# Kernel tuning notes

Hardware: AMD Instinct MI355X
Metric: run time of the kernel (lower is better)

## Reference

```python
import jax, jax.numpy as jnp
import numpy as np

B, T, C = 8, 4096, 192
HIMG, WIMG = 64, 64
NH, HS = 24, 8
MIX_DIM, DECAY_DIM = 32, 64


def _conv2d(x, w, pad):
    # x: [B, C, H, W], w: [Cout, Cin, kh, kw]
    return jax.lax.conv_general_dilated(
        x, w, (1, 1), [(pad, pad), (pad, pad)],
        dimension_numbers=('NCHW', 'OIHW', 'NCHW'))


def setup_inputs() -> dict:
    key = jax.random.key(0)
    ks = jax.random.split(key, 26)
    f = jax.random.normal
    s = 1.0 / np.sqrt(C)
    return {
        'x': f(ks[0], (B, T, C), jnp.float32),
        'maa_x': f(ks[1], (1, 1, C), jnp.float32) * 0.1,
        'maa_w': f(ks[2], (1, 1, C), jnp.float32) * 0.1,
        'maa_k': f(ks[3], (1, 1, C), jnp.float32) * 0.1,
        'maa_v': f(ks[4], (1, 1, C), jnp.float32) * 0.1,
        'maa_r': f(ks[5], (1, 1, C), jnp.float32) * 0.1,
        'maa_g': f(ks[6], (1, 1, C), jnp.float32) * 0.1,
        'maa_w1': f(ks[7], (C, 5 * MIX_DIM), jnp.float32) * 0.01,
        'maa_w2': f(ks[8], (5, MIX_DIM, C), jnp.float32) * 0.01,
        'decay_w1': f(ks[9], (C, DECAY_DIM), jnp.float32) * 0.01,
        'decay_w2': f(ks[10], (DECAY_DIM, C), jnp.float32) * 0.01,
        'spatial_decay': f(ks[11], (1, 1, C), jnp.float32) * 0.5,
        'u': f(ks[12], (NH, HS), jnp.float32) * 0.5,
        'Wr': f(ks[13], (C, C), jnp.float32) * s,
        'Wk': f(ks[14], (C, C), jnp.float32) * s,
        'Wv': f(ks[15], (C, C), jnp.float32) * s,
        'Wg': f(ks[16], (C, C), jnp.float32) * s,
        'Wo': f(ks[17], (C, C), jnp.float32) * s,
        'ln_g': jnp.ones((C,), jnp.float32),
        'ln_b': jnp.zeros((C,), jnp.float32),
        'w_lp': f(ks[18], (C, C), jnp.float32) * s,
        'w_hd': f(ks[19], (C, C, 3), jnp.float32) * s,
        'w_vd': f(ks[20], (C, C, 3), jnp.float32) * s,
        'w_cd': f(ks[21], (C, C, 3, 3), jnp.float32) * (s / 3.0),
        'theta_cd': jnp.full((1,), 0.7, jnp.float32),
    }


def _diff_conv_mix(x2d, w_lp, w_hd, w_vd, w_cd, theta_cd):
    Cc = x2d.shape[1]
    # laplacian-pattern conv from a 1x1 weight (Conv2d_lp)
    k9 = jnp.zeros((Cc, Cc, 9), x2d.dtype)
    k9 = k9.at[:, :, jnp.array([1, 3, 5, 7])].set(w_lp[:, :, None])
    k9 = k9.at[:, :, 4].set(-4.0 * w_lp)
    out = _conv2d(x2d, k9.reshape(Cc, Cc, 3, 3), 1)
    # horizontal difference conv (Conv2d_hd)
    k9 = jnp.zeros((Cc, Cc, 9), x2d.dtype)
    k9 = k9.at[:, :, jnp.array([0, 3, 6])].set(w_hd)
    k9 = k9.at[:, :, jnp.array([2, 5, 8])].set(-w_hd)
    out = out + _conv2d(x2d, k9.reshape(Cc, Cc, 3, 3), 1)
    # vertical difference conv (Conv2d_vd)
    k9 = jnp.zeros((Cc, Cc, 9), x2d.dtype)
    k9 = k9.at[:, :, jnp.array([0, 1, 2])].set(w_vd)
    k9 = k9.at[:, :, jnp.array([6, 7, 8])].set(-w_vd)
    out = out + _conv2d(x2d, k9.reshape(Cc, Cc, 3, 3), 1)
    # central difference conv (Conv2d_cd): normal conv + 1x1 (-theta * kernel sum)
    out = out + _conv2d(x2d, w_cd, 1)
    kd = jnp.sum(w_cd, axis=(2, 3), keepdims=True) * (-theta_cd[0])
    out = out + _conv2d(x2d, kd, 0)
    return out


def reference(x, maa_x, maa_w, maa_k, maa_v, maa_r, maa_g, maa_w1, maa_w2,
              decay_w1, decay_w2, spatial_decay, u, Wr, Wk, Wv, Wg, Wo,
              ln_g, ln_b, w_lp, w_hd, w_vd, w_cd, theta_cd):
    Bb, Tt, Cc = x.shape
    x2d = x.transpose(0, 2, 1).reshape(Bb, Cc, HIMG, WIMG)
    shifted = _diff_conv_mix(x2d, w_lp, w_hd, w_vd, w_cd, theta_cd)
    xx = shifted.reshape(Bb, Cc, Tt).transpose(0, 2, 1) - x  # spatial shift delta

    # data-dependent token mixing (RWKV6 maa)
    xxx = x + xx * maa_x
    tmp = jnp.tanh(xxx @ maa_w1).reshape(Bb, Tt, 5, MIX_DIM)
    m = jnp.einsum('btfd,fdc->fbtc', tmp, maa_w2)  # [5, B, T, C]
    mw, mk, mv, mr, mg = m[0], m[1], m[2], m[3], m[4]
    xw = x + xx * (maa_w + mw)
    xk = x + xx * (maa_k + mk)
    xv = x + xx * (maa_v + mv)
    xr = x + xx * (maa_r + mr)
    xg = x + xx * (maa_g + mg)

    r = xr @ Wr
    k = xk @ Wk
    v = xv @ Wv
    g = jax.nn.silu(xg @ Wg)
    w = spatial_decay + jnp.tanh(xw @ decay_w1) @ decay_w2  # [B, T, C]

    # WKV6 linear recurrence, fp32 state, per-head [HS, HS]
    rh = r.reshape(Bb, Tt, NH, HS).astype(jnp.float32)
    kh = k.reshape(Bb, Tt, NH, HS).astype(jnp.float32)
    vh = v.reshape(Bb, Tt, NH, HS).astype(jnp.float32)
    dh = jnp.exp(-jnp.exp(w.astype(jnp.float32))).reshape(Bb, Tt, NH, HS)
    uf = u.astype(jnp.float32)

    def step(S, inp):  # S: [B, NH, HS(j key), HS(i value)]
        rt, kt, vt, dt = inp  # each [B, NH, HS]
        kv = kt[..., :, None] * vt[..., None, :]
        yt = jnp.einsum('bhj,bhji->bhi', rt, S + uf[None, :, :, None] * kv)
        return dt[..., None] * S + kv, yt

    xs = tuple(a.transpose(1, 0, 2, 3) for a in (rh, kh, vh, dh))  # time-major
    S0 = jnp.zeros((Bb, NH, HS, HS), jnp.float32)
    _, ys = jax.lax.scan(step, S0, xs)
    y = ys.transpose(1, 0, 2, 3).reshape(Bb, Tt, Cc).astype(x.dtype)

    # ln_x then gated output projection
    mu = jnp.mean(y, axis=-1, keepdims=True)
    var = jnp.mean((y - mu) ** 2, axis=-1, keepdims=True)
    yn = (y - mu) * jax.lax.rsqrt(var + 1e-5) * ln_g + ln_b
    return (yn * g) @ Wo
```

## Files before the change

kernel.cpp:

```cpp
#include <hip/hip_runtime.h>
#include <hip/hip_bf16.h>

#define Bq 8
#define Tq 4096
#define Cq 192
#define NHq 24
#define HSq 8
#define Mq (Bq * Tq)

#define CLq 64
#define NCHq (Tq / CLq)
#define TSq 32

typedef short short8 __attribute__((ext_vector_type(8)));
typedef float f32x4 __attribute__((ext_vector_type(4)));

__device__ __forceinline__ unsigned short f2bf(float f) {
    union { float f; unsigned u; } v; v.f = f;
    unsigned u = v.u;
    return (unsigned short)((u + 0x7FFFu + ((u >> 16) & 1u)) >> 16);
}
__device__ __forceinline__ float bf2f(unsigned short u) {
    union { unsigned u; float f; } v; v.u = (unsigned)u << 16;
    return v.f;
}
__device__ __forceinline__ float4 bf4_to_f4(ushort4 u) {
    return make_float4(bf2f(u.x), bf2f(u.y), bf2f(u.z), bf2f(u.w));
}

__global__ void prep_weights_kernel(const float* __restrict__ w_lp,
                                    const float* __restrict__ w_hd,
                                    const float* __restrict__ w_vd,
                                    const float* __restrict__ w_cd,
                                    const float* __restrict__ theta,
                                    unsigned short* __restrict__ Wg) {
    int idx = blockIdx.x * 256 + threadIdx.x;
    if (idx >= Cq * Cq) return;
    int cout = idx / Cq, cin = idx - cout * Cq;
    float t9[9];
#pragma unroll
    for (int t = 0; t < 9; ++t) t9[t] = 0.f;
    float lp = w_lp[idx];
    t9[1] += lp; t9[3] += lp; t9[5] += lp; t9[7] += lp; t9[4] -= 4.f * lp;
    float h0 = w_hd[idx * 3 + 0], h1 = w_hd[idx * 3 + 1], h2 = w_hd[idx * 3 + 2];
    t9[0] += h0; t9[3] += h1; t9[6] += h2;
    t9[2] -= h0; t9[5] -= h1; t9[8] -= h2;
    float v0 = w_vd[idx * 3 + 0], v1 = w_vd[idx * 3 + 1], v2 = w_vd[idx * 3 + 2];
    t9[0] += v0; t9[1] += v1; t9[2] += v2;
    t9[6] -= v0; t9[7] -= v1; t9[8] -= v2;
    float sum = 0.f;
#pragma unroll
    for (int t = 0; t < 9; ++t) {
        float cdv = w_cd[idx * 9 + t];
        t9[t] += cdv; sum += cdv;
    }
    t9[4] -= theta[0] * sum;
#pragma unroll
    for (int t = 0; t < 9; ++t)
        Wg[(size_t)cout * 1728 + t * Cq + cin] = f2bf(t9[t]);
}

__global__ __launch_bounds__(256) void prep_pack_kernel(
    const float* __restrict__ maa_w1, const float* __restrict__ Wr,
    const float* __restrict__ Wk, const float* __restrict__ Wv,
    const float* __restrict__ Wgp, const float* __restrict__ Wo,
    const float* __restrict__ maa_w2, const float* __restrict__ d1,
    const float* __restrict__ d2,
    unsigned short* __restrict__ Wt_maa, unsigned short* __restrict__ Wt_r,
    unsigned short* __restrict__ Wt_k, unsigned short* __restrict__ Wt_v,
    unsigned short* __restrict__ Wt_g, unsigned short* __restrict__ Wt_o,
    unsigned short* __restrict__ w2t, unsigned short* __restrict__ Wt_d1,
    unsigned short* __restrict__ Wt_d2) {
    int idx = blockIdx.x * 256 + threadIdx.x;
    if (idx < 30720) {
        int n = idx / 192, k = idx - n * 192;
        Wt_maa[idx] = f2bf(maa_w1[(size_t)k * 160 + n]);
        return;
    }
    idx -= 30720;
    if (idx < 5 * 36864) {
        int s = idx / 36864, e = idx - s * 36864;
        int n = e / 192, k = e - n * 192;
        const float* W = s == 0 ? Wr : s == 1 ? Wk : s == 2 ? Wv : s == 3 ? Wgp : Wo;
        unsigned short* D = s == 0 ? Wt_r : s == 1 ? Wt_k : s == 2 ? Wt_v : s == 3 ? Wt_g : Wt_o;
        D[e] = f2bf(W[(size_t)k * 192 + n]);
        return;
    }
    idx -= 5 * 36864;
    if (idx < 30720) {
        int f = idx / 6144, rem = idx - f * 6144;
        int n = rem >> 5, k = rem & 31;
        w2t[idx] = f2bf(maa_w2[(size_t)(f * 32 + k) * 192 + n]);
        return;
    }
    idx -= 30720;
    if (idx < 12288) {
        int n = idx / 192, k = idx - n * 192;
        Wt_d1[idx] = f2bf(d1[(size_t)k * 64 + n]);
        return;
    }
    idx -= 12288;
    if (idx < 12288) {
        int n = idx / 64, k = idx - n * 64;
        Wt_d2[idx] = f2bf(d2[(size_t)k * 192 + n]);
    }
}

__global__ __launch_bounds__(256) void halo_kernel(
    const float* __restrict__ x, unsigned short* __restrict__ xh) {
    int idx = blockIdx.x * 256 + threadIdx.x;
    int c4 = (idx % 48) * 4;
    int cell = idx / 48;
    int hx = cell % 66;
    int rest = cell / 66;
    int hy = rest % 66;
    int bb = rest / 66;
    ushort4 o = make_ushort4(0, 0, 0, 0);
    if (hy >= 1 && hy <= 64 && hx >= 1 && hx <= 64) {
        size_t g = ((size_t)(bb << 12) + (hy - 1) * 64 + (hx - 1)) * Cq + c4;
        float4 v = *(const float4*)&x[g];
        o = make_ushort4(f2bf(v.x), f2bf(v.y), f2bf(v.z), f2bf(v.w));
    }
    *(ushort4*)&xh[(size_t)cell * Cq + c4] = o;
}

#define GBM 128
#define GBK 64

template <int ALOAD, int EPI, int OBF16, int BN>
__global__ __launch_bounds__(256) void mgemm_kernel(
    const unsigned short* __restrict__ Asrc,
    const unsigned short* __restrict__ Wt,
    void* __restrict__ Cv, int N, int K,
    const float* __restrict__ aux0,
    const unsigned short* __restrict__ xh,
    unsigned short* __restrict__ C2) {
    __shared__ unsigned char lds[(GBM + BN) * GBK * 2];
    unsigned char* Alds = lds;
    unsigned char* Blds = lds + GBM * GBK * 2;
    float* C = (float*)Cv;
    unsigned short* Cb = (unsigned short*)Cv;

    const int tid = threadIdx.x;
    const int wid = tid >> 6, lane = tid & 63;
    const int llo = lane & 15, lhi = lane >> 4;
    const int m0 = blockIdx.x * GBM, n0 = blockIdx.y * BN;
    const int NF = BN / 16;

    f32x4 acc[2][BN / 16];
#pragma unroll
    for (int a = 0; a < 2; ++a)
#pragma unroll
        for (int b = 0; b < NF; ++b) {
            f32x4 z = {0.f, 0.f, 0.f, 0.f};
            acc[a][b] = z;
        }

    for (int k0 = 0; k0 < K; k0 += GBK) {
        __syncthreads();
#pragma unroll
        for (int rep = 0; rep < 4; ++rep) {
            int c = tid + rep * 256;
            int row = c >> 3, kseg = c & 7;
            int m = m0 + row;
            short8 val;
            if (ALOAD == 3) {
                val = *(const short8*)&Asrc[(size_t)m * K + k0 + kseg * 8];
            } else {
                int tap = k0 / Cq;
                int cinb = k0 - tap * Cq;
                int t3 = tap / 3;
                int bb = m >> 12, pos = m & 4095;
                int hy = (pos >> 6) + t3;
                int hx = (pos & 63) + tap - t3 * 3;
                size_t g = ((size_t)bb * 4356 + hy * 66 + hx) * Cq + cinb + kseg * 8;
                val = *(const short8*)&Asrc[g];
            }
            *(short8*)(Alds + row * 128 + ((kseg * 16) ^ ((row & 7) << 4))) = val;
        }
#pragma unroll
        for (int rep = 0; rep < BN / 32; ++rep) {
            int c = tid + rep * 256;
            int row = c >> 3, kseg = c & 7;
            int n = n0 + row;
            short8 val = {0, 0, 0, 0, 0, 0, 0, 0};
            if (n < N) val = *(const short8*)&Wt[(size_t)n * K + k0 + kseg * 8];
            *(short8*)(Blds + row * 128 + ((kseg * 16) ^ ((row & 7) << 4))) = val;
        }
        __syncthreads();
#pragma unroll
        for (int kc = 0; kc < 2; ++kc) {
            int kb = kc * 64 + lhi * 16;
            short8 af[2], bq[BN / 16];
#pragma unroll
            for (int mf = 0; mf < 2; ++mf) {
                int row = wid * 32 + mf * 16 + llo;
                af[mf] = *(const short8*)(Alds + row * 128 + (kb ^ ((row & 7) << 4)));
            }
#pragma unroll
            for (int nf = 0; nf < NF; ++nf) {
                int row = nf * 16 + llo;
                bq[nf] = *(const short8*)(Blds + row * 128 + (kb ^ ((row & 7) << 4)));
            }
#pragma unroll
            for (int mf = 0; mf < 2; ++mf)
#pragma unroll
                for (int nf = 0; nf < NF; ++nf)
                    acc[mf][nf] = __builtin_amdgcn_mfma_f32_16x16x32_bf16(
                        af[mf], bq[nf], acc[mf][nf], 0, 0, 0);
        }
    }
    if (EPI == 5) {
#pragma unroll
        for (int mf = 0; mf < 2; ++mf)
#pragma unroll
            for (int nf = 0; nf < NF; ++nf) {
                int n = n0 + nf * 16 + llo;
#pragma unroll
                for (int r = 0; r < 4; ++r) {
                    int m = m0 + wid * 32 + mf * 16 + lhi * 4 + r;
                    int pos = m & 4095, bb = m >> 12;
                    size_t cell = (size_t)bb * 4356 + ((pos >> 6) + 1) * 66 + (pos & 63) + 1;
                    float xv = bf2f(xh[cell * Cq + n]);
                    float xxv = acc[mf][nf][r] - xv;
                    Cb[(size_t)m * Cq + n] = f2bf(xxv);
                    C2[(size_t)m * Cq + n] = f2bf(fmaf(xxv, aux0[n], xv));
                }
            }
        return;
    }
#pragma unroll
    for (int mf = 0; mf < 2; ++mf) {
#pragma unroll
        for (int nf = 0; nf < NF; ++nf) {
            int n = n0 + nf * 16 + llo;
            if (n >= N) continue;
#pragma unroll
            for (int r = 0; r < 4; ++r) {
                int m = m0 + wid * 32 + mf * 16 + lhi * 4 + r;
                float val = acc[mf][nf][r];
                if (EPI == 2) val = tanhf(val);
                else if (EPI == 4) val = expf(-expf(aux0[n] + val));
                if (OBF16) Cb[(size_t)m * N + n] = f2bf(val);
                else C[(size_t)m * N + n] = val;
            }
        }
    }
}

__global__ __launch_bounds__(256) void proj4_kernel(
    const unsigned short* __restrict__ A0, const unsigned short* __restrict__ A1,
    const unsigned short* __restrict__ A2, const unsigned short* __restrict__ A3,
    const unsigned short* __restrict__ W0, const unsigned short* __restrict__ W1,
    const unsigned short* __restrict__ W2, const unsigned short* __restrict__ W3,
    unsigned short* __restrict__ O0, unsigned short* __restrict__ O1,
    unsigned short* __restrict__ O2, unsigned short* __restrict__ O3) {
    __shared__ unsigned char lds[(GBM + 64) * GBK * 2];
    unsigned char* Alds = lds;
    unsigned char* Blds = lds + GBM * GBK * 2;
    const int z = blockIdx.z;
    const unsigned short* Asrc = z == 0 ? A0 : z == 1 ? A1 : z == 2 ? A2 : A3;
    const unsigned short* Wt = z == 0 ? W0 : z == 1 ? W1 : z == 2 ? W2 : W3;
    unsigned short* Cb = z == 0 ? O0 : z == 1 ? O1 : z == 2 ? O2 : O3;
    const bool silu = (z == 3);

    const int tid = threadIdx.x;
    const int wid = tid >> 6, lane = tid & 63;
    const int llo = lane & 15, lhi = lane >> 4;
    const int m0 = blockIdx.x * GBM, n0 = blockIdx.y * 64;

    f32x4 acc[2][4];
#pragma unroll
    for (int a = 0; a < 2; ++a)
#pragma unroll
        for (int b = 0; b < 4; ++b) {
            f32x4 zz = {0.f, 0.f, 0.f, 0.f};
            acc[a][b] = zz;
        }

    for (int k0 = 0; k0 < Cq; k0 += GBK) {
        __syncthreads();
#pragma unroll
        for (int rep = 0; rep < 4; ++rep) {
            int c = tid + rep * 256;
            int row = c >> 3, kseg = c & 7;
            short8 val = *(const short8*)&Asrc[(size_t)(m0 + row) * Cq + k0 + kseg * 8];
            *(short8*)(Alds + row * 128 + ((kseg * 16) ^ ((row & 7) << 4))) = val;
        }
#pragma unroll
        for (int rep = 0; rep < 2; ++rep) {
            int c = tid + rep * 256;
            int row = c >> 3, kseg = c & 7;
            short8 val = *(const short8*)&Wt[(size_t)(n0 + row) * Cq + k0 + kseg * 8];
            *(short8*)(Blds + row * 128 + ((kseg * 16) ^ ((row & 7) << 4))) = val;
        }
        __syncthreads();
#pragma unroll
        for (int kc = 0; kc < 2; ++kc) {
            int kb = kc * 64 + lhi * 16;
            short8 af[2], bq[4];
#pragma unroll
            for (int mf = 0; mf < 2; ++mf) {
                int row = wid * 32 + mf * 16 + llo;
                af[mf] = *(const short8*)(Alds + row * 128 + (kb ^ ((row & 7) << 4)));
            }
#pragma unroll
            for (int nf = 0; nf < 4; ++nf) {
                int row = nf * 16 + llo;
                bq[nf] = *(const short8*)(Blds + row * 128 + (kb ^ ((row & 7) << 4)));
            }
#pragma unroll
            for (int mf = 0; mf < 2; ++mf)
#pragma unroll
                for (int nf = 0; nf < 4; ++nf)
                    acc[mf][nf] = __builtin_amdgcn_mfma_f32_16x16x32_bf16(
                        af[mf], bq[nf], acc[mf][nf], 0, 0, 0);
        }
    }
#pragma unroll
    for (int mf = 0; mf < 2; ++mf)
#pragma unroll
        for (int nf = 0; nf < 4; ++nf) {
            int n = n0 + nf * 16 + llo;
#pragma unroll
            for (int r = 0; r < 4; ++r) {
                int m = m0 + wid * 32 + mf * 16 + lhi * 4 + r;
                float val = acc[mf][nf][r];
                if (silu) val = val / (1.f + expf(-val));
                Cb[(size_t)m * Cq + n] = f2bf(val);
            }
        }
}

#define MLDW 72
__global__ __launch_bounds__(128) void mix5_kernel(
    const unsigned short* __restrict__ xh,
    const unsigned short* __restrict__ xxb,
    const unsigned short* __restrict__ tmp_bf,
    const unsigned short* __restrict__ w2t,
    const float* __restrict__ maa_w, const float* __restrict__ maa_k,
    const float* __restrict__ maa_v, const float* __restrict__ maa_r,
    const float* __restrict__ maa_g,
    unsigned short* __restrict__ xw, unsigned short* __restrict__ xr,
    unsigned short* __restrict__ xk, unsigned short* __restrict__ xv,
    unsigned short* __restrict__ xg) {
    __shared__ unsigned short tile[2][5][16][MLDW];
    const int tid = threadIdx.x;
    const int wid = tid >> 6, lane = tid & 63;
    const int llo = lane & 15, lhi = lane >> 4;
    const int mb = blockIdx.x * 64 + wid * 32;
    const int nb = blockIdx.y * 64;

    short8 aw[5][4];
#pragma unroll
    for (int f = 0; f < 5; ++f)
#pragma unroll
        for (int nf = 0; nf < 4; ++nf)
            aw[f][nf] = *(const short8*)&w2t[((size_t)f * Cq + nb + nf * 16 + llo) * 32 + lhi * 8];

    unsigned short* const outs[5] = {xw, xk, xv, xr, xg};

#pragma unroll
    for (int sub = 0; sub < 2; ++sub) {
        short8 bt[5];
        {
            const unsigned short* trow = &tmp_bf[(size_t)(mb + sub * 16 + llo) * 160 + lhi * 8];
#pragma unroll
            for (int f = 0; f < 5; ++f) bt[f] = *(const short8*)&trow[f * 32];
        }
        int m = mb + sub * 16 + llo;
        int pos = m & 4095, bb = m >> 12;
        size_t xbase = ((size_t)bb * 4356 + ((pos >> 6) + 1) * 66 + (pos & 63) + 1) * Cq;
#pragma unroll
        for (int nf = 0; nf < 4; ++nf) {
            f32x4 acc[5];
#pragma unroll
            for (int f = 0; f < 5; ++f) {
                f32x4 z = {0.f, 0.f, 0.f, 0.f};
                acc[f] = __builtin_amdgcn_mfma_f32_16x16x32_bf16(aw[f][nf], bt[f], z, 0, 0, 0);
            }
            int n0 = nb + nf * 16 + lhi * 4;
            size_t g = (size_t)m * Cq + n0;
            float4 xv4 = bf4_to_f4(*(const ushort4*)&xh[xbase + n0]);
            float4 xx4 = bf4_to_f4(*(const ushort4*)&xxb[g]);
            float4 mw4 = *(const float4*)&maa_w[n0];
            float4 mk4 = *(const float4*)&maa_k[n0];
            float4 mv4 = *(const float4*)&maa_v[n0];
            float4 mr4 = *(const float4*)&maa_r[n0];
            float4 mg4 = *(const float4*)&maa_g[n0];
            float xvv[4] = {xv4.x, xv4.y, xv4.z, xv4.w};
            float xxv[4] = {xx4.x, xx4.y, xx4.z, xx4.w};
            float mwv[4] = {mw4.x, mw4.y, mw4.z, mw4.w};
            float mkv[4] = {mk4.x, mk4.y, mk4.z, mk4.w};
            float mvv[4] = {mv4.x, mv4.y, mv4.z, mv4.w};
            float mrv[4] = {mr4.x, mr4.y, mr4.z, mr4.w};
            float mgv[4] = {mg4.x, mg4.y, mg4.z, mg4.w};
            ushort4 ov[5];
#pragma unroll
            for (int r = 0; r < 4; ++r) {
                ((unsigned short*)&ov[0])[r] = f2bf(fmaf(xxv[r], mwv[r] + acc[0][r], xvv[r]));
                ((unsigned short*)&ov[1])[r] = f2bf(fmaf(xxv[r], mkv[r] + acc[1][r], xvv[r]));
                ((unsigned short*)&ov[2])[r] = f2bf(fmaf(xxv[r], mvv[r] + acc[2][r], xvv[r]));
                ((unsigned short*)&ov[3])[r] = f2bf(fmaf(xxv[r], mrv[r] + acc[3][r], xvv[r]));
                ((unsigned short*)&ov[4])[r] = f2bf(fmaf(xxv[r], mgv[r] + acc[4][r], xvv[r]));
            }
            int col = nf * 16 + lhi * 4;
#pragma unroll
            for (int f = 0; f < 5; ++f)
                *(ushort4*)&tile[wid][f][llo][col] = ov[f];
        }
        int row16 = lane >> 3;
        int colc = (lane & 7) * 8;
#pragma unroll
        for (int f = 0; f < 5; ++f) {
#pragma unroll
            for (int p = 0; p < 2; ++p) {
                int rr = p * 8 + row16;
                int gm = mb + sub * 16 + rr;
                *(short8*)&outs[f][(size_t)gm * Cq + nb + colc] =
                    *(const short8*)&tile[wid][f][rr][colc];
            }
        }
    }
}

__global__ __launch_bounds__(64) void wkv_pass1_kernel(
    const unsigned short* __restrict__ k, const unsigned short* __restrict__ v,
    const float* __restrict__ d,
    float* __restrict__ Dbuf, float* __restrict__ Cbuf) {
    int chunk = blockIdx.x, hg = blockIdx.y, b = blockIdx.z;
    int lane = threadIdx.x;
    int slot = lane >> 3, i = lane & 7;
    int cbase = hg * 64;
    size_t gbase = ((size_t)b * Tq + (size_t)chunk * CLq) * Cq + cbase;
    __shared__ float ks[TSq][64], vs[TSq][64], ds[TSq][64];
    float S[8], D[8];
#pragma unroll
    for (int j = 0; j < 8; ++j) { S[j] = 0.f; D[j] = 1.f; }
    for (int t0 = 0; t0 < CLq; t0 += TSq) {
        int f = lane & 15, r4 = lane >> 4;
#pragma unroll
        for (int p = 0; p < 8; ++p) {
            int row = r4 + p * 4;
            size_t g = gbase + (size_t)(t0 + row) * Cq + f * 4;
            *(float4*)&ks[row][f * 4] = bf4_to_f4(*(const ushort4*)&k[g]);
            *(float4*)&vs[row][f * 4] = bf4_to_f4(*(const ushort4*)&v[g]);
            *(float4*)&ds[row][f * 4] = *(const float4*)&d[g];
        }
        __syncthreads();
#pragma unroll 8
        for (int t = 0; t < TSq; ++t) {
            float vv = vs[t][lane];
            float4 ka = *(const float4*)&ks[t][slot * 8];
            float4 kb = *(const float4*)&ks[t][slot * 8 + 4];
            float4 da = *(const float4*)&ds[t][slot * 8];
            float4 db = *(const float4*)&ds[t][slot * 8 + 4];
            float kk[8] = {ka.x, ka.y, ka.z, ka.w, kb.x, kb.y, kb.z, kb.w};
            float dd[8] = {da.x, da.y, da.z, da.w, db.x, db.y, db.z, db.w};
#pragma unroll
            for (int j = 0; j < 8; ++j) {
                float kv = kk[j] * vv;
                S[j] = fmaf(dd[j], S[j], kv);
                D[j] *= dd[j];
            }
        }
        __syncthreads();
    }
    size_t dbase = (((size_t)b * NCHq + chunk) * NHq + hg * 8) * 8;
    Dbuf[dbase + lane] = D[i];
    size_t cb = (((size_t)b * NCHq + chunk) * NHq + (hg * 8 + slot)) * 64 + i;
#pragma unroll
    for (int j = 0; j < 8; ++j) Cbuf[cb + j * 8] = S[j];
}

__global__ __launch_bounds__(64) void wkv_pass2_kernel(
    const float* __restrict__ Dbuf, const float* __restrict__ Cbuf,
    float* __restrict__ Sbuf) {
    int bh = blockIdx.x;
    int lane = threadIdx.x;
    int j = lane >> 3, i = lane & 7;
    int b = bh / NHq, h = bh - b * NHq;
    float S = 0.f;
    size_t stride = (size_t)NHq * 64;
    size_t base = ((size_t)b * NCHq * NHq + h) * 64 + j * 8 + i;
    size_t dstride = (size_t)NHq * 8;
    size_t dbase = ((size_t)b * NCHq * NHq + h) * 8 + j;
#pragma unroll 4
    for (int c = 0; c < NCHq; ++c) {
        Sbuf[base + c * stride] = S;
        float D = Dbuf[dbase + c * dstride];
        float C = Cbuf[base + c * stride];
        S = fmaf(D, S, C);
    }
}

__global__ __launch_bounds__(64) void wkv_pass3_kernel(
    const unsigned short* __restrict__ r, const unsigned short* __restrict__ k,
    const unsigned short* __restrict__ v, const float* __restrict__ d,
    const float* __restrict__ u, const float* __restrict__ Sbuf,
    unsigned short* __restrict__ y) {
    int chunk = blockIdx.x, hg = blockIdx.y, b = blockIdx.z;
    int lane = threadIdx.x;
    int slot = lane >> 3, i = lane & 7;
    int h = hg * 8 + slot;
    int cbase = hg * 64;
    size_t gbase = ((size_t)b * Tq + (size_t)chunk * CLq) * Cq + cbase;
    __shared__ float rs[TSq][64], ks[TSq][64], vs[TSq][64], ds[TSq][64];
    float S[8], uu[8];
    size_t sb = (((size_t)b * NCHq + chunk) * NHq + h) * 64 + i;
#pragma unroll
    for (int j = 0; j < 8; ++j) {
        S[j] = Sbuf[sb + j * 8];
        uu[j] = u[h * 8 + j];
    }
    for (int t0 = 0; t0 < CLq; t0 += TSq) {
        int f = lane & 15, r4 = lane >> 4;
#pragma unroll
        for (int p = 0; p < 8; ++p) {
            int row = r4 + p * 4;
            size_t g = gbase + (size_t)(t0 + row) * Cq + f * 4;
            *(float4*)&rs[row][f * 4] = bf4_to_f4(*(const ushort4*)&r[g]);
            *(float4*)&ks[row][f * 4] = bf4_to_f4(*(const ushort4*)&k[g]);
            *(float4*)&vs[row][f * 4] = bf4_to_f4(*(const ushort4*)&v[g]);
            *(float4*)&ds[row][f * 4] = *(const float4*)&d[g];
        }
        __syncthreads();
#pragma unroll 8
        for (int t = 0; t < TSq; ++t) {
            float vv = vs[t][lane];
            float4 ra = *(const float4*)&rs[t][slot * 8];
            float4 rb = *(const float4*)&rs[t][slot * 8 + 4];
            float4 ka = *(const float4*)&ks[t][slot * 8];
            float4 kb = *(const float4*)&ks[t][slot * 8 + 4];
            float4 da = *(const float4*)&ds[t][slot * 8];
            float4 db = *(const float4*)&ds[t][slot * 8 + 4];
            float rr[8] = {ra.x, ra.y, ra.z, ra.w, rb.x, rb.y, rb.z, rb.w};
            float kk[8] = {ka.x, ka.y, ka.z, ka.w, kb.x, kb.y, kb.z, kb.w};
            float dd[8] = {da.x, da.y, da.z, da.w, db.x, db.y, db.z, db.w};
            float yv = 0.f;
#pragma unroll
            for (int j = 0; j < 8; ++j) {
                float kv = kk[j] * vv;
                yv = fmaf(rr[j], fmaf(uu[j], kv, S[j]), yv);
                S[j] = fmaf(dd[j], S[j], kv);
            }
            y[gbase + (size_t)(t0 + t) * Cq + lane] = f2bf(yv);
        }
        __syncthreads();
    }
}

__global__ __launch_bounds__(256) void ln_gate_kernel(
    const unsigned short* __restrict__ y, const unsigned short* __restrict__ g,
    const float* __restrict__ ln_g, const float* __restrict__ ln_b,
    unsigned short* __restrict__ out) {
    int row = blockIdx.x * 4 + (threadIdx.x >> 6);
    int lane = threadIdx.x & 63;
    const unsigned short* yr = y + (size_t)row * Cq;
    float a0 = bf2f(yr[lane]), a1 = bf2f(yr[lane + 64]), a2 = bf2f(yr[lane + 128]);
    float s = a0 + a1 + a2;
    float ss = a0 * a0 + a1 * a1 + a2 * a2;
#pragma unroll
    for (int m = 1; m < 64; m <<= 1) {
        s += __shfl_xor(s, m);
        ss += __shfl_xor(ss, m);
    }
    float mu = s * (1.f / 192.f);
    float var = ss * (1.f / 192.f) - mu * mu;
    float rstd = rsqrtf(var + 1e-5f);
    const unsigned short* gr = g + (size_t)row * Cq;
    unsigned short* orow = out + (size_t)row * Cq;
    float aa[3] = {a0, a1, a2};
#pragma unroll
    for (int q = 0; q < 3; ++q) {
        int cc = lane + q * 64;
        float yn = (aa[q] - mu) * rstd * ln_g[cc] + ln_b[cc];
        orow[cc] = f2bf(yn * bf2f(gr[cc]));
    }
}

extern "C" void kernel_launch(void* const* d_in, const int* in_sizes, int n_in,
                              void* d_out, int out_size, void* d_ws, size_t ws_size,
                              hipStream_t stream) {
    const float* x        = (const float*)d_in[0];
    const float* maa_x    = (const float*)d_in[1];
    const float* maa_w    = (const float*)d_in[2];
    const float* maa_k    = (const float*)d_in[3];
    const float* maa_v    = (const float*)d_in[4];
    const float* maa_r    = (const float*)d_in[5];
    const float* maa_g    = (const float*)d_in[6];
    const float* maa_w1   = (const float*)d_in[7];
    const float* maa_w2   = (const float*)d_in[8];
    const float* decay_w1 = (const float*)d_in[9];
    const float* decay_w2 = (const float*)d_in[10];
    const float* sdecay   = (const float*)d_in[11];
    const float* u        = (const float*)d_in[12];
    const float* Wr       = (const float*)d_in[13];
    const float* Wk       = (const float*)d_in[14];
    const float* Wv       = (const float*)d_in[15];
    const float* Wgp      = (const float*)d_in[16];
    const float* Wo       = (const float*)d_in[17];
    const float* ln_g     = (const float*)d_in[18];
    const float* ln_b     = (const float*)d_in[19];
    const float* w_lp     = (const float*)d_in[20];
    const float* w_hd     = (const float*)d_in[21];
    const float* w_vd     = (const float*)d_in[22];
    const float* w_cd     = (const float*)d_in[23];
    const float* theta    = (const float*)d_in[24];
    float* out = (float*)d_out;

    const size_t BIG = (size_t)Mq * Cq;
    float* ws = (float*)d_ws;
    unsigned short* Wgt_conv = (unsigned short*)ws;
    unsigned short* Wt_maa = Wgt_conv + (size_t)Cq * 1728;
    unsigned short* Wt_r = Wt_maa + 160 * Cq;
    unsigned short* Wt_k = Wt_r + Cq * Cq;
    unsigned short* Wt_v = Wt_k + Cq * Cq;
    unsigned short* Wt_g = Wt_v + Cq * Cq;
    unsigned short* Wt_o = Wt_g + Cq * Cq;
    unsigned short* w2t  = Wt_o + Cq * Cq;
    unsigned short* Wt_d1 = w2t + 5 * 192 * 32;
    unsigned short* Wt_d2 = Wt_d1 + 64 * Cq;
    float* tmp  = ws + 331776;
    float* wtmp = tmp + (size_t)Mq * 160;
    float* buf0 = wtmp + (size_t)Mq * 64;
    float* buf1 = buf0 + BIG;
    float* buf2 = buf1 + BIG;
    float* buf3 = buf2 + BIG;
    float* buf4 = buf3 + BIG;
    float* buf5 = buf4 + BIG;

    unsigned short* tmp_bf = (unsigned short*)tmp;
    float* Dbuf = tmp + (size_t)Mq * 80;
    float* Cbuf = Dbuf + (size_t)Bq * NCHq * NHq * 8;
    float* Sbuf = Cbuf + (size_t)Bq * NCHq * NHq * 64;

    unsigned short* x_halo = (unsigned short*)buf1;
    unsigned short* y_b    = (unsigned short*)buf1;
    unsigned short* k_b    = (unsigned short*)(buf1 + BIG / 2);
    unsigned short* xx_b   = (unsigned short*)buf0;
    unsigned short* xw_b   = (unsigned short*)(buf0 + BIG / 2);
    unsigned short* r_b    = (unsigned short*)buf0;
    unsigned short* xxx_b  = (unsigned short*)(buf2 + BIG / 2);
    unsigned short* xg_b   = xxx_b;
    unsigned short* xv_b   = (unsigned short*)buf2;
    unsigned short* gate_b = (unsigned short*)buf2;
    unsigned short* v_b    = (unsigned short*)buf3;
    unsigned short* g_b    = (unsigned short*)buf4;
    unsigned short* xr_b   = (unsigned short*)buf5;
    unsigned short* xk_b   = (unsigned short*)(buf5 + BIG / 2);
    float* d_f             = buf5;
    unsigned short* wtmp_b = (unsigned short*)wtmp;

    dim3 blk(256);
    const unsigned short* nosrc = nullptr;
    unsigned short* nodst = nullptr;

    prep_weights_kernel<<<dim3(144), blk, 0, stream>>>(w_lp, w_hd, w_vd, w_cd, theta, Wgt_conv);
    prep_pack_kernel<<<dim3(1056), blk, 0, stream>>>(
        maa_w1, Wr, Wk, Wv, Wgp, Wo, maa_w2, decay_w1, decay_w2,
        Wt_maa, Wt_r, Wt_k, Wt_v, Wt_g, Wt_o, w2t, Wt_d1, Wt_d2);
    halo_kernel<<<dim3(8 * 66 * 66 * 48 / 256), blk, 0, stream>>>(x, x_halo);
    mgemm_kernel<1, 5, 1, 96><<<dim3(Mq / GBM, 2), blk, 0, stream>>>(
        x_halo, Wgt_conv, xx_b, Cq, 1728, maa_x, x_halo, xxx_b);
    mgemm_kernel<3, 2, 1, 64><<<dim3(Mq / GBM, 3), blk, 0, stream>>>(
        xxx_b, Wt_maa, tmp_bf, 160, Cq, nullptr, nosrc, nodst);
    mix5_kernel<<<dim3(Mq / 64, 3), dim3(128), 0, stream>>>(
        x_halo, xx_b, tmp_bf, w2t, maa_w, maa_k, maa_v, maa_r, maa_g,
        xw_b, xr_b, xk_b, xv_b, xg_b);
    proj4_kernel<<<dim3(Mq / GBM, 3, 4), blk, 0, stream>>>(
        xv_b, xr_b, xk_b, xg_b,
        Wt_v, Wt_r, Wt_k, Wt_g,
        v_b, r_b, k_b, g_b);
    mgemm_kernel<3, 2, 1, 64><<<dim3(Mq / GBM, 1), blk, 0, stream>>>(
        xw_b, Wt_d1, wtmp_b, 64, Cq, nullptr, nosrc, nodst);
    mgemm_kernel<3, 4, 0, 64><<<dim3(Mq / GBM, 3), blk, 0, stream>>>(
        wtmp_b, Wt_d2, d_f, Cq, 64, sdecay, nosrc, nodst);
    wkv_pass1_kernel<<<dim3(NCHq, 3, Bq), dim3(64), 0, stream>>>(k_b, v_b, d_f, Dbuf, Cbuf);
    wkv_pass2_kernel<<<dim3(Bq * NHq), dim3(64), 0, stream>>>(Dbuf, Cbuf, Sbuf);
    wkv_pass3_kernel<<<dim3(NCHq, 3, Bq), dim3(64), 0, stream>>>(r_b, k_b, v_b, d_f, u, Sbuf, y_b);
    ln_gate_kernel<<<dim3(Mq / 4), blk, 0, stream>>>(y_b, g_b, ln_g, ln_b, gate_b);
    mgemm_kernel<3, 0, 0, 64><<<dim3(Mq / GBM, 3), blk, 0, stream>>>(
        gate_b, Wt_o, out, Cq, Cq, nullptr, nosrc, nodst);
}
```

Before: 329.1 us.

## Load GEMM A fragments directly from global; keep bf16 in WKV shared memory

The GEMM kernels (mgemm and proj4) no longer stage the A tile through LDS. Each wave loads its MFMA A fragments straight from global memory into registers, and only the weight tile stays in shared memory. The conv GEMM drops its BN=96 template variant and runs as a 3-column grid of 64-wide N tiles. The WKV pass1 and pass3 kernels now keep r, k and v as bf16 in LDS and convert at use, halving their shared-memory footprint and store traffic. The aims are less LDS traffic, fewer LDS stores and better occupancy, at the risk of less coalesced global loads for A and more A re-reads across N tiles.

```diff
diff --git a/kernel.cpp b/kernel.cpp
--- a/kernel.cpp
+++ b/kernel.cpp
@@ -127,7 +127,7 @@
 #define GBM 128
 #define GBK 64
 
-template <int ALOAD, int EPI, int OBF16, int BN>
+template <int ALOAD, int EPI, int OBF16>
 __global__ __launch_bounds__(256) void mgemm_kernel(
     const unsigned short* __restrict__ Asrc,
     const unsigned short* __restrict__ Wt,
@@ -135,23 +135,20 @@
     const float* __restrict__ aux0,
     const unsigned short* __restrict__ xh,
     unsigned short* __restrict__ C2) {
-    __shared__ unsigned char lds[(GBM + BN) * GBK * 2];
-    unsigned char* Alds = lds;
-    unsigned char* Blds = lds + GBM * GBK * 2;
+    __shared__ unsigned char Blds[64 * GBK * 2];
     float* C = (float*)Cv;
     unsigned short* Cb = (unsigned short*)Cv;
 
     const int tid = threadIdx.x;
     const int wid = tid >> 6, lane = tid & 63;
     const int llo = lane & 15, lhi = lane >> 4;
-    const int m0 = blockIdx.x * GBM, n0 = blockIdx.y * BN;
-    const int NF = BN / 16;
-
-    f32x4 acc[2][BN / 16];
+    const int m0 = blockIdx.x * GBM, n0 = blockIdx.y * 64;
+
+    f32x4 acc[2][4];
 #pragma unroll
     for (int a = 0; a < 2; ++a)
 #pragma unroll
-        for (int b = 0; b < NF; ++b) {
+        for (int b = 0; b < 4; ++b) {
             f32x4 z = {0.f, 0.f, 0.f, 0.f};
             acc[a][b] = z;
         }
@@ -159,27 +156,7 @@
     for (int k0 = 0; k0 < K; k0 += GBK) {
         __syncthreads();
 #pragma unroll
-        for (int rep = 0; rep < 4; ++rep) {
-            int c = tid + rep * 256;
-            int row = c >> 3, kseg = c & 7;
-            int m = m0 + row;
-            short8 val;
-            if (ALOAD == 3) {
-                val = *(const short8*)&Asrc[(size_t)m * K + k0 + kseg * 8];
-            } else {
-                int tap = k0 / Cq;
-                int cinb = k0 - tap * Cq;
-                int t3 = tap / 3;
-                int bb = m >> 12, pos = m & 4095;
-                int hy = (pos >> 6) + t3;
-                int hx = (pos & 63) + tap - t3 * 3;
-                size_t g = ((size_t)bb * 4356 + hy * 66 + hx) * Cq + cinb + kseg * 8;
-                val = *(const short8*)&Asrc[g];
-            }
-            *(short8*)(Alds + row * 128 + ((kseg * 16) ^ ((row & 7) << 4))) = val;
-        }
-#pragma unroll
-        for (int rep = 0; rep < BN / 32; ++rep) {
+        for (int rep = 0; rep < 2; ++rep) {
             int c = tid + rep * 256;
             int row = c >> 3, kseg = c & 7;
             int n = n0 + row;
@@ -187,34 +164,49 @@
             if (n < N) val = *(const short8*)&Wt[(size_t)n * K + k0 + kseg * 8];
             *(short8*)(Blds + row * 128 + ((kseg * 16) ^ ((row & 7) << 4))) = val;
         }
+        short8 af[2][2];
+#pragma unroll
+        for (int mf = 0; mf < 2; ++mf) {
+            int row = m0 + wid * 32 + mf * 16 + llo;
+            size_t base;
+            if (ALOAD == 3) {
+                base = (size_t)row * K + k0;
+            } else {
+                int tap = k0 / Cq;
+                int cinb = k0 - tap * Cq;
+                int t3 = tap / 3;
+                int bb = row >> 12, pos = row & 4095;
+                int hy = (pos >> 6) + t3;
+                int hx = (pos & 63) + tap - t3 * 3;
+                base = ((size_t)bb * 4356 + hy * 66 + hx) * Cq + cinb;
+            }
+#pragma unroll
+            for (int kc = 0; kc < 2; ++kc)
+                af[mf][kc] = *(const short8*)&Asrc[base + kc * 32 + lhi * 8];
+        }
         __syncthreads();
 #pragma unroll
         for (int kc = 0; kc < 2; ++kc) {
             int kb = kc * 64 + lhi * 16;
-            short8 af[2], bq[BN / 16];
-#pragma unroll
-            for (int mf = 0; mf < 2; ++mf) {
-                int row = wid * 32 + mf * 16 + llo;
-                af[mf] = *(const short8*)(Alds + row * 128 + (kb ^ ((row & 7) << 4)));
-            }
-#pragma unroll
-            for (int nf = 0; nf < NF; ++nf) {
+            short8 bq[4];
+#pragma unroll
+            for (int nf = 0; nf < 4; ++nf) {
                 int row = nf * 16 + llo;
                 bq[nf] = *(const short8*)(Blds + row * 128 + (kb ^ ((row & 7) << 4)));
             }
 #pragma unroll
             for (int mf = 0; mf < 2; ++mf)
 #pragma unroll
-                for (int nf = 0; nf < NF; ++nf)
+                for (int nf = 0; nf < 4; ++nf)
                     acc[mf][nf] = __builtin_amdgcn_mfma_f32_16x16x32_bf16(
-                        af[mf], bq[nf], acc[mf][nf], 0, 0, 0);
+                        af[mf][kc], bq[nf], acc[mf][nf], 0, 0, 0);
         }
     }
     if (EPI == 5) {
 #pragma unroll
         for (int mf = 0; mf < 2; ++mf)
 #pragma unroll
-            for (int nf = 0; nf < NF; ++nf) {
+            for (int nf = 0; nf < 4; ++nf) {
                 int n = n0 + nf * 16 + llo;
 #pragma unroll
                 for (int r = 0; r < 4; ++r) {
@@ -232,7 +224,7 @@
 #pragma unroll
     for (int mf = 0; mf < 2; ++mf) {
 #pragma unroll
-        for (int nf = 0; nf < NF; ++nf) {
+        for (int nf = 0; nf < 4; ++nf) {
             int n = n0 + nf * 16 + llo;
             if (n >= N) continue;
 #pragma unroll
@@ -255,9 +247,7 @@
     const unsigned short* __restrict__ W2, const unsigned short* __restrict__ W3,
     unsigned short* __restrict__ O0, unsigned short* __restrict__ O1,
     unsigned short* __restrict__ O2, unsigned short* __restrict__ O3) {
-    __shared__ unsigned char lds[(GBM + 64) * GBK * 2];
-    unsigned char* Alds = lds;
-    unsigned char* Blds = lds + GBM * GBK * 2;
+    __shared__ unsigned char Blds[64 * GBK * 2];
     const int z = blockIdx.z;
     const unsigned short* Asrc = z == 0 ? A0 : z == 1 ? A1 : z == 2 ? A2 : A3;
     const unsigned short* Wt = z == 0 ? W0 : z == 1 ? W1 : z == 2 ? W2 : W3;
@@ -281,29 +271,25 @@
     for (int k0 = 0; k0 < Cq; k0 += GBK) {
         __syncthreads();
 #pragma unroll
-        for (int rep = 0; rep < 4; ++rep) {
-            int c = tid + rep * 256;
-            int row = c >> 3, kseg = c & 7;
-            short8 val = *(const short8*)&Asrc[(size_t)(m0 + row) * Cq + k0 + kseg * 8];
-            *(short8*)(Alds + row * 128 + ((kseg * 16) ^ ((row & 7) << 4))) = val;
-        }
-#pragma unroll
         for (int rep = 0; rep < 2; ++rep) {
             int c = tid + rep * 256;
             int row = c >> 3, kseg = c & 7;
             short8 val = *(const short8*)&Wt[(size_t)(n0 + row) * Cq + k0 + kseg * 8];
             *(short8*)(Blds + row * 128 + ((kseg * 16) ^ ((row & 7) << 4))) = val;
         }
+        short8 af[2][2];
+#pragma unroll
+        for (int mf = 0; mf < 2; ++mf) {
+            size_t base = (size_t)(m0 + wid * 32 + mf * 16 + llo) * Cq + k0;
+#pragma unroll
+            for (int kc = 0; kc < 2; ++kc)
+                af[mf][kc] = *(const short8*)&Asrc[base + kc * 32 + lhi * 8];
+        }
         __syncthreads();
 #pragma unroll
         for (int kc = 0; kc < 2; ++kc) {
             int kb = kc * 64 + lhi * 16;
-            short8 af[2], bq[4];
-#pragma unroll
-            for (int mf = 0; mf < 2; ++mf) {
-                int row = wid * 32 + mf * 16 + llo;
-                af[mf] = *(const short8*)(Alds + row * 128 + (kb ^ ((row & 7) << 4)));
-            }
+            short8 bq[4];
 #pragma unroll
             for (int nf = 0; nf < 4; ++nf) {
                 int row = nf * 16 + llo;
@@ -314,7 +300,7 @@
 #pragma unroll
                 for (int nf = 0; nf < 4; ++nf)
                     acc[mf][nf] = __builtin_amdgcn_mfma_f32_16x16x32_bf16(
-                        af[mf], bq[nf], acc[mf][nf], 0, 0, 0);
+                        af[mf][kc], bq[nf], acc[mf][nf], 0, 0, 0);
         }
     }
 #pragma unroll
@@ -433,7 +419,8 @@
     int slot = lane >> 3, i = lane & 7;
     int cbase = hg * 64;
     size_t gbase = ((size_t)b * Tq + (size_t)chunk * CLq) * Cq + cbase;
-    __shared__ float ks[TSq][64], vs[TSq][64], ds[TSq][64];
+    __shared__ unsigned short ks[TSq][64], vs[TSq][64];
+    __shared__ float ds[TSq][64];
     float S[8], D[8];
 #pragma unroll
     for (int j = 0; j < 8; ++j) { S[j] = 0.f; D[j] = 1.f; }
@@ -443,23 +430,21 @@
         for (int p = 0; p < 8; ++p) {
             int row = r4 + p * 4;
             size_t g = gbase + (size_t)(t0 + row) * Cq + f * 4;
-            *(float4*)&ks[row][f * 4] = bf4_to_f4(*(const ushort4*)&k[g]);
-            *(float4*)&vs[row][f * 4] = bf4_to_f4(*(const ushort4*)&v[g]);
+            *(ushort4*)&ks[row][f * 4] = *(const ushort4*)&k[g];
+            *(ushort4*)&vs[row][f * 4] = *(const ushort4*)&v[g];
             *(float4*)&ds[row][f * 4] = *(const float4*)&d[g];
         }
         __syncthreads();
 #pragma unroll 8
         for (int t = 0; t < TSq; ++t) {
-            float vv = vs[t][lane];
-            float4 ka = *(const float4*)&ks[t][slot * 8];
-            float4 kb = *(const float4*)&ks[t][slot * 8 + 4];
+            float vv = bf2f(vs[t][lane]);
+            short8 k8 = *(const short8*)&ks[t][slot * 8];
             float4 da = *(const float4*)&ds[t][slot * 8];
             float4 db = *(const float4*)&ds[t][slot * 8 + 4];
-            float kk[8] = {ka.x, ka.y, ka.z, ka.w, kb.x, kb.y, kb.z, kb.w};
             float dd[8] = {da.x, da.y, da.z, da.w, db.x, db.y, db.z, db.w};
 #pragma unroll
             for (int j = 0; j < 8; ++j) {
-                float kv = kk[j] * vv;
+                float kv = bf2f((unsigned short)k8[j]) * vv;
                 S[j] = fmaf(dd[j], S[j], kv);
                 D[j] *= dd[j];
             }
@@ -505,7 +490,8 @@
     int h = hg * 8 + slot;
     int cbase = hg * 64;
     size_t gbase = ((size_t)b * Tq + (size_t)chunk * CLq) * Cq + cbase;
-    __shared__ float rs[TSq][64], ks[TSq][64], vs[TSq][64], ds[TSq][64];
+    __shared__ unsigned short rs[TSq][64], ks[TSq][64], vs[TSq][64];
+    __shared__ float ds[TSq][64];
     float S[8], uu[8];
     size_t sb = (((size_t)b * NCHq + chunk) * NHq + h) * 64 + i;
 #pragma unroll
@@ -519,29 +505,25 @@
         for (int p = 0; p < 8; ++p) {
             int row = r4 + p * 4;
             size_t g = gbase + (size_t)(t0 + row) * Cq + f * 4;
-            *(float4*)&rs[row][f * 4] = bf4_to_f4(*(const ushort4*)&r[g]);
-            *(float4*)&ks[row][f * 4] = bf4_to_f4(*(const ushort4*)&k[g]);
-            *(float4*)&vs[row][f * 4] = bf4_to_f4(*(const ushort4*)&v[g]);
+            *(ushort4*)&rs[row][f * 4] = *(const ushort4*)&r[g];
+            *(ushort4*)&ks[row][f * 4] = *(const ushort4*)&k[g];
+            *(ushort4*)&vs[row][f * 4] = *(const ushort4*)&v[g];
             *(float4*)&ds[row][f * 4] = *(const float4*)&d[g];
         }
         __syncthreads();
 #pragma unroll 8
         for (int t = 0; t < TSq; ++t) {
-            float vv = vs[t][lane];
-            float4 ra = *(const float4*)&rs[t][slot * 8];
-            float4 rb = *(const float4*)&rs[t][slot * 8 + 4];
-            float4 ka = *(const float4*)&ks[t][slot * 8];
-            float4 kb = *(const float4*)&ks[t][slot * 8 + 4];
+            float vv = bf2f(vs[t][lane]);
+            short8 r8 = *(const short8*)&rs[t][slot * 8];
+            short8 k8 = *(const short8*)&ks[t][slot * 8];
             float4 da = *(const float4*)&ds[t][slot * 8];
             float4 db = *(const float4*)&ds[t][slot * 8 + 4];
-            float rr[8] = {ra.x, ra.y, ra.z, ra.w, rb.x, rb.y, rb.z, rb.w};
-            float kk[8] = {ka.x, ka.y, ka.z, ka.w, kb.x, kb.y, kb.z, kb.w};
             float dd[8] = {da.x, da.y, da.z, da.w, db.x, db.y, db.z, db.w};
             float yv = 0.f;
 #pragma unroll
             for (int j = 0; j < 8; ++j) {
-                float kv = kk[j] * vv;
-                yv = fmaf(rr[j], fmaf(uu[j], kv, S[j]), yv);
+                float kv = bf2f((unsigned short)k8[j]) * vv;
+                yv = fmaf(bf2f((unsigned short)r8[j]), fmaf(uu[j], kv, S[j]), yv);
                 S[j] = fmaf(dd[j], S[j], kv);
             }
             y[gbase + (size_t)(t0 + t) * Cq + lane] = f2bf(yv);
@@ -661,9 +643,9 @@
         maa_w1, Wr, Wk, Wv, Wgp, Wo, maa_w2, decay_w1, decay_w2,
         Wt_maa, Wt_r, Wt_k, Wt_v, Wt_g, Wt_o, w2t, Wt_d1, Wt_d2);
     halo_kernel<<<dim3(8 * 66 * 66 * 48 / 256), blk, 0, stream>>>(x, x_halo);
-    mgemm_kernel<1, 5, 1, 96><<<dim3(Mq / GBM, 2), blk, 0, stream>>>(
+    mgemm_kernel<1, 5, 1><<<dim3(Mq / GBM, 3), blk, 0, stream>>>(
         x_halo, Wgt_conv, xx_b, Cq, 1728, maa_x, x_halo, xxx_b);
-    mgemm_kernel<3, 2, 1, 64><<<dim3(Mq / GBM, 3), blk, 0, stream>>>(
+    mgemm_kernel<3, 2, 1><<<dim3(Mq / GBM, 3), blk, 0, stream>>>(
         xxx_b, Wt_maa, tmp_bf, 160, Cq, nullptr, nosrc, nodst);
     mix5_kernel<<<dim3(Mq / 64, 3), dim3(128), 0, stream>>>(
         x_halo, xx_b, tmp_bf, w2t, maa_w, maa_k, maa_v, maa_r, maa_g,
@@ -672,14 +654,14 @@
         xv_b, xr_b, xk_b, xg_b,
         Wt_v, Wt_r, Wt_k, Wt_g,
         v_b, r_b, k_b, g_b);
-    mgemm_kernel<3, 2, 1, 64><<<dim3(Mq / GBM, 1), blk, 0, stream>>>(
+    mgemm_kernel<3, 2, 1><<<dim3(Mq / GBM, 1), blk, 0, stream>>>(
         xw_b, Wt_d1, wtmp_b, 64, Cq, nullptr, nosrc, nodst);
-    mgemm_kernel<3, 4, 0, 64><<<dim3(Mq / GBM, 3), blk, 0, stream>>>(
+    mgemm_kernel<3, 4, 0><<<dim3(Mq / GBM, 3), blk, 0, stream>>>(
         wtmp_b, Wt_d2, d_f, Cq, 64, sdecay, nosrc, nodst);
     wkv_pass1_kernel<<<dim3(NCHq, 3, Bq), dim3(64), 0, stream>>>(k_b, v_b, d_f, Dbuf, Cbuf);
     wkv_pass2_kernel<<<dim3(Bq * NHq), dim3(64), 0, stream>>>(Dbuf, Cbuf, Sbuf);
     wkv_pass3_kernel<<<dim3(NCHq, 3, Bq), dim3(64), 0, stream>>>(r_b, k_b, v_b, d_f, u, Sbuf, y_b);
     ln_gate_kernel<<<dim3(Mq / 4), blk, 0, stream>>>(y_b, g_b, ln_g, ln_b, gate_b);
-    mgemm_kernel<3, 0, 0, 64><<<dim3(Mq / GBM, 3), blk, 0, stream>>>(
+    mgemm_kernel<3, 0, 0><<<dim3(Mq / GBM, 3), blk, 0, stream>>>(
         gate_b, Wt_o, out, Cq, Cq, nullptr, nosrc, nodst);
 }
```

After: 337.6 us. +2.6%, slower.
